# Performance work log

Hardware: AMD Instinct MI355X
Metric: run time of the kernel (lower is better)

Reference implementation:

```python
import jax, jax.numpy as jnp
import numpy as np

N, E, DIM, H, T, R = 50000, 400000, 128, 8, 4, 6
D = DIM // H  # head dim = 16


def setup_inputs() -> dict:
    key = jax.random.key(0)
    ks = jax.random.split(key, 12)
    s = 0.1
    return {
        "x": jax.random.normal(ks[0], (N, DIM), jnp.float32),
        "src": jax.random.randint(ks[1], (E,), 0, N),
        "dst": jax.random.randint(ks[2], (E,), 0, N),
        "ntype": jax.random.randint(ks[3], (N,), 0, T),
        "etype": jax.random.randint(ks[4], (E,), 0, R),
        # TypedLinear weights: [num_types, in, out] (no bias in DGL TypedLinear)
        "Wk": jax.random.normal(ks[5], (T, DIM, DIM), jnp.float32) * s,
        "Wq": jax.random.normal(ks[6], (T, DIM, DIM), jnp.float32) * s,
        "Wv": jax.random.normal(ks[7], (T, DIM, DIM), jnp.float32) * s,
        "Wa": jax.random.normal(ks[8], (T, DIM, DIM), jnp.float32) * s,
        # relation_pri[h][r], relation_att/msg: per-head per-etype [D,D]
        "rel_pri": jnp.ones((H, R), jnp.float32) + jax.random.normal(ks[9], (H, R), jnp.float32) * 0.1,
        "rel_att": jax.random.normal(ks[10], (H, R, D, D), jnp.float32) * 0.25,
        "rel_msg": jax.random.normal(ks[11], (H, R, D, D), jnp.float32) * 0.25,
        "skip": jnp.ones((T,), jnp.float32),  # sigmoid-gated skip per node type
        "ln_gamma": jnp.ones((DIM,), jnp.float32),
        "ln_beta": jnp.zeros((DIM,), jnp.float32),
    }


def _typed_linear(x, W, types):
    # x: [N, in], W: [Ttypes, in, out], types: [N] -> y_i = x_i @ W[types_i]
    out = jnp.zeros((x.shape[0], W.shape[-1]), x.dtype)
    for t in range(W.shape[0]):
        out = jnp.where((types == t)[:, None], x @ W[t], out)
    return out


def _typed_rel(xe, W, etype):
    # xe: [E, H, D], W: [H, Rtypes, D, D] -> y_e[h] = xe_e[h] @ W[h, etype_e]
    out = jnp.zeros_like(xe)
    for r in range(W.shape[1]):
        yr = jnp.einsum('ehd,hdo->eho', xe, W[:, r])
        out = jnp.where((etype == r)[:, None, None], yr, out)
    return out


def reference(x, src, dst, ntype, etype, Wk, Wq, Wv, Wa, rel_pri, rel_att, rel_msg, skip, ln_gamma, ln_beta):
    # ---- HGTConv ----
    k = _typed_linear(x, Wk, ntype).reshape(N, H, D)
    q = _typed_linear(x, Wq, ntype).reshape(N, H, D)
    v = _typed_linear(x, Wv, ntype).reshape(N, H, D)
    k_e = k[src]   # [E,H,D]
    q_e = q[dst]
    v_e = v[src]
    kw = _typed_rel(k_e, rel_att, etype)                       # [E,H,D]
    a = (kw * q_e).sum(-1) * rel_pri.T[etype] / jnp.sqrt(jnp.float32(D))  # [E,H]
    m = _typed_rel(v_e, rel_msg, etype)                        # [E,H,D]
    # edge softmax over incoming edges per dst node, per head
    amax = jax.lax.stop_gradient(jax.ops.segment_max(a, dst, num_segments=N))
    amax = jnp.where(jnp.isfinite(amax), amax, 0.0)
    ex = jnp.exp(a - amax[dst])
    den = jax.ops.segment_sum(ex, dst, num_segments=N)
    attn = ex / jnp.maximum(den[dst], 1e-9)                    # [E,H]
    h = jax.ops.segment_sum(m * attn[:, :, None], dst, num_segments=N).reshape(N, DIM)
    h = _typed_linear(h, Wa, ntype)  # dropout = identity (eval mode)
    gate = jax.nn.sigmoid(skip)[ntype][:, None]
    h = h * gate + x * (1.0 - gate)  # in_dim == out_dim -> identity skip path
    # ---- RelationAwareLayer tail: Identity residual + dropout(identity) + LayerNorm ----
    y = x + h
    mu = y.mean(-1, keepdims=True)
    var = ((y - mu) ** 2).mean(-1, keepdims=True)
    return (y - mu) / jnp.sqrt(var + 1e-5) * ln_gamma + ln_beta
```

## Files before the change

### kernel.cpp

```cpp
#include <hip/hip_runtime.h>
#include <math.h>

#define N_NODES 50000
#define N_EDGES 400000
#define H_HEADS 8
#define D_HEAD 16
#define R_TYPES 6
#define T_TYPES 4
#define DIM 128
#define BN 16
#define MAX_TILES ((N_NODES + BN - 1) / BN + T_TYPES)
#define NKEYS (N_NODES * R_TYPES)
#define NBLK_K ((NKEYS + 255) / 256)
#define NBLK_N ((N_NODES + 255) / 256)
#define SM_SHIFT 8.0f

typedef unsigned short bf16_t;

__device__ __forceinline__ float bf2f(bf16_t u) {
    unsigned int v = ((unsigned int)u) << 16;
    return __int_as_float((int)v);
}
__device__ __forceinline__ bf16_t f2bf(float f) {
    unsigned int u = (unsigned int)__float_as_int(f);
    unsigned int lsb = (u >> 16) & 1u;
    u += 0x7fffu + lsb;
    return (bf16_t)(u >> 16);
}
__device__ __forceinline__ void bf2x(unsigned int u, float& a, float& b) {
    a = bf2f((bf16_t)(u & 0xffffu));
    b = bf2f((bf16_t)(u >> 16));
}
__device__ __forceinline__ unsigned int pk(float a, float b) {
    return (unsigned int)f2bf(a) | ((unsigned int)f2bf(b) << 16);
}


__global__ void k_scanA(const int* __restrict__ cnt, int* __restrict__ offs,
                        int* __restrict__ partial, int n) {
    __shared__ int tmp[256];
    int tid = threadIdx.x;
    int i = blockIdx.x * 256 + tid;
    int v = (i < n) ? cnt[i] : 0;
    tmp[tid] = v;
    __syncthreads();
    for (int o = 1; o < 256; o <<= 1) {
        int t = (tid >= o) ? tmp[tid - o] : 0;
        __syncthreads();
        tmp[tid] += t;
        __syncthreads();
    }
    if (i < n) offs[i] = tmp[tid] - v;
    if (tid == 255) partial[blockIdx.x] = tmp[255];
}

__global__ void k_rscan(int* __restrict__ a, int total) {
    __shared__ int tmp[256];
    __shared__ int carry_s;
    int tid = threadIdx.x;
    if (tid == 0) carry_s = 0;
    __syncthreads();
    for (int base = 0; base < total; base += 256) {
        int i = base + tid;
        int v = (i < total) ? a[i] : 0;
        tmp[tid] = v;
        __syncthreads();
        for (int o = 1; o < 256; o <<= 1) {
            int t = (tid >= o) ? tmp[tid - o] : 0;
            __syncthreads();
            tmp[tid] += t;
            __syncthreads();
        }
        int carry = carry_s;
        if (i < total) a[i] = carry + tmp[tid] - v;
        __syncthreads();
        if (tid == 255) carry_s = carry + tmp[255];
        __syncthreads();
    }
}

__global__ void k_scanC2(int* __restrict__ offs, const int* __restrict__ partial,
                         int* __restrict__ cursor, int n) {
    int i = blockIdx.x * 256 + threadIdx.x;
    if (i < n) {
        int v = offs[i] + partial[blockIdx.x];
        offs[i] = v;
        cursor[i] = v;
    }
}


__global__ void k_count6(const int* __restrict__ srcA, const int* __restrict__ etype,
                         int* __restrict__ deg6, int n) {
    int e = blockIdx.x * blockDim.x + threadIdx.x;
    if (e < n) atomicAdd(&deg6[etype[e] * N_NODES + srcA[e]], 1);
}

__global__ void k_countD(const int* __restrict__ dst, int* __restrict__ degD, int n) {
    int e = blockIdx.x * blockDim.x + threadIdx.x;
    if (e < n) atomicAdd(&degD[dst[e]], 1);
}

__global__ void k_scatter6(const int* __restrict__ src, const int* __restrict__ dst,
                           const int* __restrict__ etype, int* __restrict__ cursor6,
                           int* __restrict__ esrc_s, int* __restrict__ edst_s, int n) {
    int e = blockIdx.x * blockDim.x + threadIdx.x;
    if (e < n) {
        int key = etype[e] * N_NODES + src[e];
        int pos = atomicAdd(&cursor6[key], 1);
        esrc_s[pos] = src[e];
        edst_s[pos] = dst[e];
    }
}

__global__ void k_dpos(const int* __restrict__ edst_s, int* __restrict__ cursorD,
                       int* __restrict__ dpos, int n) {
    int p = blockIdx.x * blockDim.x + threadIdx.x;
    if (p < n) dpos[p] = atomicAdd(&cursorD[edst_s[p]], 1);
}


__global__ void k_tcount_agg(const int* __restrict__ ntype, int* __restrict__ tcnt,
                             int* __restrict__ wpos, int n) {
    __shared__ int hist[T_TYPES];
    __shared__ int base[T_TYPES];
    int tid = threadIdx.x;
    if (tid < T_TYPES) hist[tid] = 0;
    __syncthreads();
    int i = blockIdx.x * 256 + tid;
    int t = 0, rank = 0;
    if (i < n) {
        t = ntype[i];
        rank = atomicAdd(&hist[t], 1);
    }
    __syncthreads();
    if (tid < T_TYPES)
        base[tid] = (hist[tid] > 0) ? atomicAdd(&tcnt[tid], hist[tid]) : 0;
    __syncthreads();
    if (i < n) wpos[i] = base[t] + rank;
}

__global__ void k_tsetup(const int* __restrict__ tcnt, int* __restrict__ pbase,
                         int* __restrict__ ntiles_g, int* __restrict__ tile_type) {
    __shared__ int off[T_TYPES + 1];
    if (threadIdx.x == 0) {
        int o = 0;
        for (int t = 0; t < T_TYPES; ++t) {
            off[t] = o;
            pbase[t] = o * BN;
            o += (tcnt[t] + BN - 1) / BN;
        }
        off[T_TYPES] = o;
        *ntiles_g = o;
    }
    __syncthreads();
    int total = off[T_TYPES];
    for (int i = threadIdx.x; i < total; i += blockDim.x) {
        int t = 0;
        while (t < T_TYPES - 1 && i >= off[t + 1]) ++t;
        tile_type[i] = t;
    }
}

__global__ void k_tscatter2(const int* __restrict__ ntype, const int* __restrict__ wpos,
                            const int* __restrict__ pbase, int* __restrict__ nlist, int n) {
    int i = blockIdx.x * 256 + threadIdx.x;
    if (i < n) nlist[pbase[ntype[i]] + wpos[i]] = i;
}


__global__ __launch_bounds__(192) void k_kqv_gemm4(
    const float* __restrict__ x, const int* __restrict__ nlist,
    const int* __restrict__ tile_type, const int* __restrict__ ntiles_g,
    const float* __restrict__ Wk, const float* __restrict__ Wq,
    const float* __restrict__ Wv,
    bf16_t* __restrict__ kb, bf16_t* __restrict__ qb, bf16_t* __restrict__ vb) {
    __shared__ float xs[BN][DIM];
    __shared__ int sids[BN];
    int b = blockIdx.x;
    if (b >= *ntiles_g) return;
    int tid = threadIdx.x;
    if (tid < BN) sids[tid] = nlist[b * BN + tid];
    __syncthreads();
    for (int idx = tid; idx < BN * (DIM / 4); idx += 192) {
        int row = idx >> 5;
        int q4 = idx & 31;
        int nid = sids[row];
        float4 v4 = make_float4(0.f, 0.f, 0.f, 0.f);
        if (nid >= 0) v4 = *(const float4*)(x + (size_t)nid * DIM + q4 * 4);
        *(float4*)(&xs[row][q4 * 4]) = v4;
    }
    __syncthreads();
    int lt = tid / 96;
    int wi = tid % 96;
    int mat = wi >> 5;
    int colq = wi & 31;
    int t = tile_type[b];
    const float* W = (mat == 0 ? Wk : (mat == 1 ? Wq : Wv))
                     + (size_t)t * DIM * DIM + colq * 4;
    float acc[8][4];
#pragma unroll
    for (int n = 0; n < 8; ++n) {
        acc[n][0] = 0.f; acc[n][1] = 0.f; acc[n][2] = 0.f; acc[n][3] = 0.f;
    }
    const float* xbase = &xs[lt * 8][0];
    for (int dq = 0; dq < 32; ++dq) {
        float4 w0 = *(const float4*)(W + (size_t)(dq * 4 + 0) * DIM);
        float4 w1 = *(const float4*)(W + (size_t)(dq * 4 + 1) * DIM);
        float4 w2 = *(const float4*)(W + (size_t)(dq * 4 + 2) * DIM);
        float4 w3 = *(const float4*)(W + (size_t)(dq * 4 + 3) * DIM);
#pragma unroll
        for (int n = 0; n < 8; ++n) {
            float4 xv = *(const float4*)(xbase + n * DIM + dq * 4);
            acc[n][0] = fmaf(xv.x, w0.x, acc[n][0]);
            acc[n][0] = fmaf(xv.y, w1.x, acc[n][0]);
            acc[n][0] = fmaf(xv.z, w2.x, acc[n][0]);
            acc[n][0] = fmaf(xv.w, w3.x, acc[n][0]);
            acc[n][1] = fmaf(xv.x, w0.y, acc[n][1]);
            acc[n][1] = fmaf(xv.y, w1.y, acc[n][1]);
            acc[n][1] = fmaf(xv.z, w2.y, acc[n][1]);
            acc[n][1] = fmaf(xv.w, w3.y, acc[n][1]);
            acc[n][2] = fmaf(xv.x, w0.z, acc[n][2]);
            acc[n][2] = fmaf(xv.y, w1.z, acc[n][2]);
            acc[n][2] = fmaf(xv.z, w2.z, acc[n][2]);
            acc[n][2] = fmaf(xv.w, w3.z, acc[n][2]);
            acc[n][3] = fmaf(xv.x, w0.w, acc[n][3]);
            acc[n][3] = fmaf(xv.y, w1.w, acc[n][3]);
            acc[n][3] = fmaf(xv.z, w2.w, acc[n][3]);
            acc[n][3] = fmaf(xv.w, w3.w, acc[n][3]);
        }
    }
    bf16_t* ob = (mat == 0 ? kb : (mat == 1 ? qb : vb));
#pragma unroll
    for (int n = 0; n < 8; ++n) {
        int nid = sids[lt * 8 + n];
        if (nid >= 0) {
            ushort4 o4;
            o4.x = f2bf(acc[n][0]); o4.y = f2bf(acc[n][1]);
            o4.z = f2bf(acc[n][2]); o4.w = f2bf(acc[n][3]);
            *(ushort4*)(ob + (size_t)nid * DIM + colq * 4) = o4;
        }
    }
}


__global__ __launch_bounds__(256) void k_edge_m(
    const bf16_t* __restrict__ kbuf, const bf16_t* __restrict__ qbuf,
    const bf16_t* __restrict__ vbuf,
    const int* __restrict__ esrc_s, const int* __restrict__ edst_s,
    const int* __restrict__ beg6, const int* __restrict__ dpos,
    const float* __restrict__ rel_att, const float* __restrict__ rel_msg,
    const float* __restrict__ rel_pri,
    float* __restrict__ ex_out, bf16_t* __restrict__ m_out, int nE) {
    __shared__ float A2[2][8 * 260];
    __shared__ float M2[2][8 * 260];
    __shared__ float pri[2][8];
    __shared__ int rb_s[R_TYPES + 1];
    __shared__ int r01[2];
    int b = blockIdx.x;
    int e0 = b * 32;
    int tid = threadIdx.x;
    int nHere = nE - e0; if (nHere > 32) nHere = 32;
    if (nHere <= 0) return;
    if (tid < R_TYPES) rb_s[tid] = beg6[tid * N_NODES];
    if (tid == R_TYPES) rb_s[R_TYPES] = nE;
    __syncthreads();
    if (tid == 0) {
        int rA = 0, rB = 0;
        int eL = e0 + nHere - 1;
#pragma unroll
        for (int r = 1; r < R_TYPES; ++r) {
            if (e0 >= rb_s[r]) rA = r;
            if (eL >= rb_s[r]) rB = r;
        }
        r01[0] = rA; r01[1] = rB;
    }
    __syncthreads();
    int r0 = r01[0], r1 = r01[1];
    int bnd = rb_s[r0 + 1];
    for (int idx = tid; idx < 2 * 2048; idx += 256) {
        int slot = idx >> 11;
        if (slot == 1 && r1 == r0) break;
        int rem = idx & 2047;
        int h = rem >> 8, dj = rem & 255;
        int rr = slot ? r1 : r0;
        A2[slot][h * 260 + dj] = rel_att[(h * R_TYPES + rr) * 256 + dj];
        M2[slot][h * 260 + dj] = rel_msg[(h * R_TYPES + rr) * 256 + dj];
    }
    if (tid < 16) {
        int slot = tid >> 3, h = tid & 7;
        pri[slot][h] = rel_pri[h * R_TYPES + (slot ? r1 : r0)] * 0.25f;
    }
    __syncthreads();
    int el = tid >> 3;
    int h  = tid & 7;
    int q2 = e0 + el;
    if (q2 >= nE) return;
    int s = esrc_s[q2], dn = edst_s[q2];
    int slot = (q2 >= bnd) ? 1 : 0;
    const uint4* kp = (const uint4*)(kbuf + (size_t)s  * DIM + h * 16);
    const uint4* qp = (const uint4*)(qbuf + (size_t)dn * DIM + h * 16);
    const uint4* vp = (const uint4*)(vbuf + (size_t)s  * DIM + h * 16);
    uint4 ka = kp[0], kb4 = kp[1];
    uint4 qa = qp[0], qb4 = qp[1];
    uint4 va = vp[0], vb4 = vp[1];
    float kk[16], qq[16], vv[16];
    bf2x(ka.x,  kk[0],  kk[1]);  bf2x(ka.y,  kk[2],  kk[3]);
    bf2x(ka.z,  kk[4],  kk[5]);  bf2x(ka.w,  kk[6],  kk[7]);
    bf2x(kb4.x, kk[8],  kk[9]);  bf2x(kb4.y, kk[10], kk[11]);
    bf2x(kb4.z, kk[12], kk[13]); bf2x(kb4.w, kk[14], kk[15]);
    bf2x(qa.x,  qq[0],  qq[1]);  bf2x(qa.y,  qq[2],  qq[3]);
    bf2x(qa.z,  qq[4],  qq[5]);  bf2x(qa.w,  qq[6],  qq[7]);
    bf2x(qb4.x, qq[8],  qq[9]);  bf2x(qb4.y, qq[10], qq[11]);
    bf2x(qb4.z, qq[12], qq[13]); bf2x(qb4.w, qq[14], qq[15]);
    bf2x(va.x,  vv[0],  vv[1]);  bf2x(va.y,  vv[2],  vv[3]);
    bf2x(va.z,  vv[4],  vv[5]);  bf2x(va.w,  vv[6],  vv[7]);
    bf2x(vb4.x, vv[8],  vv[9]);  bf2x(vb4.y, vv[10], vv[11]);
    bf2x(vb4.z, vv[12], vv[13]); bf2x(vb4.w, vv[14], vv[15]);

    const float4* A4 = (const float4*)&A2[slot][h * 260];
    float accj[16];
#pragma unroll
    for (int j = 0; j < 16; ++j) accj[j] = 0.f;
#pragma unroll
    for (int d = 0; d < 16; ++d) {
        float kd = kk[d];
#pragma unroll
        for (int jj = 0; jj < 4; ++jj) {
            float4 a4 = A4[d * 4 + jj];
            accj[jj * 4 + 0] = fmaf(kd, a4.x, accj[jj * 4 + 0]);
            accj[jj * 4 + 1] = fmaf(kd, a4.y, accj[jj * 4 + 1]);
            accj[jj * 4 + 2] = fmaf(kd, a4.z, accj[jj * 4 + 2]);
            accj[jj * 4 + 3] = fmaf(kd, a4.w, accj[jj * 4 + 3]);
        }
    }
    float a = 0.f;
#pragma unroll
    for (int j = 0; j < 16; ++j) a = fmaf(accj[j], qq[j], a);
    float ex = __expf(a * pri[slot][h] - SM_SHIFT);

    const float4* M4 = (const float4*)&M2[slot][h * 260];
    float mj[16];
#pragma unroll
    for (int j = 0; j < 16; ++j) mj[j] = 0.f;
#pragma unroll
    for (int d = 0; d < 16; ++d) {
        float vd = vv[d];
#pragma unroll
        for (int jj = 0; jj < 4; ++jj) {
            float4 m4 = M4[d * 4 + jj];
            mj[jj * 4 + 0] = fmaf(vd, m4.x, mj[jj * 4 + 0]);
            mj[jj * 4 + 1] = fmaf(vd, m4.y, mj[jj * 4 + 1]);
            mj[jj * 4 + 2] = fmaf(vd, m4.z, mj[jj * 4 + 2]);
            mj[jj * 4 + 3] = fmaf(vd, m4.w, mj[jj * 4 + 3]);
        }
    }
    int dp = dpos[q2];
    ex_out[(size_t)dp * 8 + h] = ex;
    uint4 o0, o1;
    o0.x = pk(ex * mj[0],  ex * mj[1]);  o0.y = pk(ex * mj[2],  ex * mj[3]);
    o0.z = pk(ex * mj[4],  ex * mj[5]);  o0.w = pk(ex * mj[6],  ex * mj[7]);
    o1.x = pk(ex * mj[8],  ex * mj[9]);  o1.y = pk(ex * mj[10], ex * mj[11]);
    o1.z = pk(ex * mj[12], ex * mj[13]); o1.w = pk(ex * mj[14], ex * mj[15]);
    uint4* op = (uint4*)(m_out + (size_t)dp * DIM + h * 16);
    op[0] = o0; op[1] = o1;
}


__global__ __launch_bounds__(256) void k_agg_stream(
    const bf16_t* __restrict__ m_out, const float* __restrict__ ex_out,
    const int* __restrict__ doffD, const int* __restrict__ degD,
    float* __restrict__ hacc, int n) {
    int tid = threadIdx.x;
    int nb = tid >> 7;
    int lane2 = tid & 127;
    int node = blockIdx.x * 2 + nb;
    if (node >= n) return;
    int h = lane2 >> 4;
    int off = doffD[node];
    int dg  = degD[node];
    float acc = 0.f, den = 0.f;
#pragma unroll 4
    for (int j = 0; j < dg; ++j) {
        den += ex_out[(size_t)(off + j) * 8 + h];
        acc += bf2f(m_out[(size_t)(off + j) * DIM + lane2]);
    }
    hacc[(size_t)node * DIM + lane2] = acc / fmaxf(den, 1e-9f);
}


__global__ __launch_bounds__(256) void k_final_gemm(
    const float* __restrict__ x, const int* __restrict__ nlist,
    const int* __restrict__ tile_type, const int* __restrict__ ntiles_g,
    const float* __restrict__ Wa, const float* __restrict__ skip,
    const float* __restrict__ gamma, const float* __restrict__ beta,
    float* __restrict__ out) {
    __shared__ float hs[BN][DIM];
    __shared__ float ys[BN][DIM];
    __shared__ int sids[BN];
    __shared__ float mred[BN], ired[BN];
    int b = blockIdx.x;
    if (b >= *ntiles_g) return;
    int tid = threadIdx.x;
    if (tid < BN) sids[tid] = nlist[b * BN + tid];
    __syncthreads();
    for (int idx = tid; idx < BN * DIM; idx += 256) {
        int row = idx >> 7, col = idx & 127;
        int nid = sids[row];
        hs[row][col] = (nid >= 0) ? out[(size_t)nid * DIM + col] : 0.f;
    }
    __syncthreads();
    int t = tile_type[b];
    int half = tid >> 7, col = tid & 127;
    const float* W = Wa + (size_t)t * DIM * DIM;
    float acc[8];
#pragma unroll
    for (int n = 0; n < 8; ++n) acc[n] = 0.f;
#pragma unroll 4
    for (int d = 0; d < DIM; ++d) {
        float w = W[d * DIM + col];
#pragma unroll
        for (int n = 0; n < 8; ++n) acc[n] = fmaf(hs[half * 8 + n][d], w, acc[n]);
    }
    float gte = 1.f / (1.f + __expf(-skip[t]));
#pragma unroll
    for (int n = 0; n < 8; ++n) {
        int row = half * 8 + n;
        int nid = sids[row];
        float xv = (nid >= 0) ? x[(size_t)nid * DIM + col] : 0.f;
        ys[row][col] = xv * (2.f - gte) + acc[n] * gte;
    }
    __syncthreads();
    int ng = tid >> 4, l16 = tid & 15;
    float s = 0.f, s2 = 0.f;
#pragma unroll
    for (int k2 = 0; k2 < 8; ++k2) {
        float yv = ys[ng][l16 + 16 * k2];
        s += yv; s2 += yv * yv;
    }
#pragma unroll
    for (int m = 1; m < 16; m <<= 1) {
        s  += __shfl_xor(s, m, 64);
        s2 += __shfl_xor(s2, m, 64);
    }
    if (l16 == 0) {
        float mu = s * (1.f / DIM);
        float var = s2 * (1.f / DIM) - mu * mu;
        mred[ng] = mu;
        ired[ng] = rsqrtf(var + 1e-5f);
    }
    __syncthreads();
    float gm = gamma[col], bt = beta[col];
#pragma unroll
    for (int n = 0; n < 8; ++n) {
        int row = half * 8 + n;
        int nid = sids[row];
        if (nid >= 0)
            out[(size_t)nid * DIM + col] = (ys[row][col] - mred[row]) * ired[row] * gm + bt;
    }
}


extern "C" void kernel_launch(void* const* d_in, const int* in_sizes, int n_in,
                              void* d_out, int out_size, void* d_ws, size_t ws_size,
                              hipStream_t stream) {
    const float* x       = (const float*)d_in[0];
    const int*   src     = (const int*)d_in[1];
    const int*   dst     = (const int*)d_in[2];
    const int*   ntype   = (const int*)d_in[3];
    const int*   etype   = (const int*)d_in[4];
    const float* Wk      = (const float*)d_in[5];
    const float* Wq      = (const float*)d_in[6];
    const float* Wv      = (const float*)d_in[7];
    const float* Wa      = (const float*)d_in[8];
    const float* rel_pri = (const float*)d_in[9];
    const float* rel_att = (const float*)d_in[10];
    const float* rel_msg = (const float*)d_in[11];
    const float* skip    = (const float*)d_in[12];
    const float* gamma   = (const float*)d_in[13];
    const float* beta    = (const float*)d_in[14];
    float* out = (float*)d_out;

    const int N = N_NODES, E = N_EDGES;

    char* ws = (char*)d_ws;
    float* ex_out = (float*)ws;
    int* deg6    = (int*)(ex_out + (size_t)E * H_HEADS);
    int* beg6    = deg6 + NKEYS;
    int* cursor6 = beg6 + NKEYS;
    int* partial6 = cursor6 + NKEYS;
    int* degD    = partial6 + NBLK_K;
    int* doffD   = degD + N;
    int* cursorD = doffD + N;
    int* partialD = cursorD + N;
    int* dpos    = partialD + NBLK_N;
    int* esrc_s  = dpos + E;
    int* edst_s  = esrc_s + E;
    int* tcnt    = edst_s + E;
    int* pbase   = tcnt + T_TYPES;
    int* ntiles  = pbase + T_TYPES;
    int* tile_type = ntiles + 1;
    int* nlist   = tile_type + MAX_TILES;
    int* wpos    = nlist + (size_t)MAX_TILES * BN;
    bf16_t* kb   = (bf16_t*)(wpos + N);
    bf16_t* qb   = kb + (size_t)N * DIM;
    bf16_t* vb   = qb + (size_t)N * DIM;
    bf16_t* m_out = vb + (size_t)N * DIM;

    const int nbE = (E + 255) / 256;

    hipMemsetAsync(deg6, 0, (size_t)NKEYS * sizeof(int), stream);
    hipMemsetAsync(degD, 0, (size_t)N * sizeof(int), stream);
    k_count6<<<nbE, 256, 0, stream>>>(src, etype, deg6, E);
    k_countD<<<nbE, 256, 0, stream>>>(dst, degD, E);
    k_scanA<<<NBLK_K, 256, 0, stream>>>(deg6, beg6, partial6, NKEYS);
    k_rscan<<<1, 256, 0, stream>>>(partial6, NBLK_K);
    k_scanC2<<<NBLK_K, 256, 0, stream>>>(beg6, partial6, cursor6, NKEYS);
    k_scanA<<<NBLK_N, 256, 0, stream>>>(degD, doffD, partialD, N);
    k_rscan<<<1, 256, 0, stream>>>(partialD, NBLK_N);
    k_scanC2<<<NBLK_N, 256, 0, stream>>>(doffD, partialD, cursorD, N);
    k_scatter6<<<nbE, 256, 0, stream>>>(
        src, dst, etype, cursor6, esrc_s, edst_s, E);
    k_dpos<<<nbE, 256, 0, stream>>>(edst_s, cursorD, dpos, E);

    hipMemsetAsync(tcnt, 0, T_TYPES * sizeof(int), stream);
    k_tcount_agg<<<NBLK_N, 256, 0, stream>>>(ntype, tcnt, wpos, N);
    k_tsetup<<<1, 256, 0, stream>>>(tcnt, pbase, ntiles, tile_type);
    hipMemsetAsync(nlist, 0xFF, (size_t)MAX_TILES * BN * sizeof(int), stream);
    k_tscatter2<<<NBLK_N, 256, 0, stream>>>(ntype, wpos, pbase, nlist, N);

    k_kqv_gemm4<<<MAX_TILES, 192, 0, stream>>>(
        x, nlist, tile_type, ntiles, Wk, Wq, Wv, kb, qb, vb);

    k_edge_m<<<(E + 31) / 32, 256, 0, stream>>>(
        kb, qb, vb, esrc_s, edst_s, beg6, dpos,
        rel_att, rel_msg, rel_pri, ex_out, m_out, E);

    k_agg_stream<<<(N + 1) / 2, 256, 0, stream>>>(
        m_out, ex_out, doffD, degD, out, N);

    k_final_gemm<<<MAX_TILES, 256, 0, stream>>>(
        x, nlist, tile_type, ntiles, Wa, skip, gamma, beta, out);
}
```

Measured before the change: 387.5 us.

## Pad per-relation edge segments to 32 so each edge block has one relation

Edges sorted by relation type are now laid out with each relation's segment padded to a multiple of 32, so every 32-edge block in the edge kernel covers a single relation. This removes the dual-slot shared-memory staging of relation matrices, the boundary search against beg6, and the per-edge slot selection. In exchange it adds two small setup kernels, memsets of the padded index arrays, up to 192 extra padded slots, and guards on negative indices in the dpos and edge kernels.

Result: slower. 396.8 us (+2.4%).

```diff
diff --git a/kernel.cpp b/kernel.cpp
--- a/kernel.cpp
+++ b/kernel.cpp
@@ -13,6 +13,7 @@
 #define NKEYS (N_NODES * R_TYPES)
 #define NBLK_K ((NKEYS + 255) / 256)
 #define NBLK_N ((N_NODES + 255) / 256)
+#define EPAD_MAX (N_EDGES + R_TYPES * 32)
 #define SM_SHIFT 8.0f
 
 typedef unsigned short bf16_t;
@@ -79,6 +80,11 @@
     }
 }
 
+__global__ void k_scanC(int* __restrict__ offs, const int* __restrict__ partial, int n) {
+    int i = blockIdx.x * 256 + threadIdx.x;
+    if (i < n) offs[i] += partial[blockIdx.x];
+}
+
 __global__ void k_scanC2(int* __restrict__ offs, const int* __restrict__ partial,
                          int* __restrict__ cursor, int n) {
     int i = blockIdx.x * 256 + threadIdx.x;
@@ -99,6 +105,30 @@
 __global__ void k_countD(const int* __restrict__ dst, int* __restrict__ degD, int n) {
     int e = blockIdx.x * blockDim.x + threadIdx.x;
     if (e < n) atomicAdd(&degD[dst[e]], 1);
+}
+
+__global__ void k_padsetup(const int* __restrict__ beg6, int* __restrict__ rb_pad,
+                           int* __restrict__ rstart, int nE) {
+    if (threadIdx.x == 0 && blockIdx.x == 0) {
+        int o = 0;
+        for (int r = 0; r < R_TYPES; ++r) {
+            int st = beg6[r * N_NODES];
+            rstart[r] = st;
+            int en = (r < R_TYPES - 1) ? beg6[(r + 1) * N_NODES] : nE;
+            rb_pad[r] = o;
+            o += (en - st + 31) & ~31;
+        }
+        rb_pad[R_TYPES] = o;
+    }
+}
+
+__global__ void k_cursor_pad(const int* __restrict__ beg6, const int* __restrict__ rb_pad,
+                             const int* __restrict__ rstart, int* __restrict__ cursor6, int n) {
+    int i = blockIdx.x * 256 + threadIdx.x;
+    if (i < n) {
+        int r = i / N_NODES;
+        cursor6[i] = rb_pad[r] + (beg6[i] - rstart[r]);
+    }
 }
 
 __global__ void k_scatter6(const int* __restrict__ src, const int* __restrict__ dst,
@@ -116,7 +146,10 @@
 __global__ void k_dpos(const int* __restrict__ edst_s, int* __restrict__ cursorD,
                        int* __restrict__ dpos, int n) {
     int p = blockIdx.x * blockDim.x + threadIdx.x;
-    if (p < n) dpos[p] = atomicAdd(&cursorD[edst_s[p]], 1);
+    if (p < n) {
+        int dn = edst_s[p];
+        if (dn >= 0) dpos[p] = atomicAdd(&cursorD[dn], 1);
+    }
 }
 
 
@@ -244,60 +277,42 @@
 }
 
 
-__global__ __launch_bounds__(256) void k_edge_m(
+__global__ __launch_bounds__(256) void k_edge_m2(
     const bf16_t* __restrict__ kbuf, const bf16_t* __restrict__ qbuf,
     const bf16_t* __restrict__ vbuf,
     const int* __restrict__ esrc_s, const int* __restrict__ edst_s,
-    const int* __restrict__ beg6, const int* __restrict__ dpos,
+    const int* __restrict__ rb_pad, const int* __restrict__ dpos,
     const float* __restrict__ rel_att, const float* __restrict__ rel_msg,
     const float* __restrict__ rel_pri,
-    float* __restrict__ ex_out, bf16_t* __restrict__ m_out, int nE) {
-    __shared__ float A2[2][8 * 260];
-    __shared__ float M2[2][8 * 260];
-    __shared__ float pri[2][8];
-    __shared__ int rb_s[R_TYPES + 1];
-    __shared__ int r01[2];
+    float* __restrict__ ex_out, bf16_t* __restrict__ m_out) {
+    __shared__ float A2[8 * 260];
+    __shared__ float M2[8 * 260];
+    __shared__ float pri[8];
+    __shared__ int r_s;
     int b = blockIdx.x;
     int e0 = b * 32;
     int tid = threadIdx.x;
-    int nHere = nE - e0; if (nHere > 32) nHere = 32;
-    if (nHere <= 0) return;
-    if (tid < R_TYPES) rb_s[tid] = beg6[tid * N_NODES];
-    if (tid == R_TYPES) rb_s[R_TYPES] = nE;
-    __syncthreads();
     if (tid == 0) {
-        int rA = 0, rB = 0;
-        int eL = e0 + nHere - 1;
-#pragma unroll
-        for (int r = 1; r < R_TYPES; ++r) {
-            if (e0 >= rb_s[r]) rA = r;
-            if (eL >= rb_s[r]) rB = r;
-        }
-        r01[0] = rA; r01[1] = rB;
-    }
-    __syncthreads();
-    int r0 = r01[0], r1 = r01[1];
-    int bnd = rb_s[r0 + 1];
-    for (int idx = tid; idx < 2 * 2048; idx += 256) {
-        int slot = idx >> 11;
-        if (slot == 1 && r1 == r0) break;
-        int rem = idx & 2047;
-        int h = rem >> 8, dj = rem & 255;
-        int rr = slot ? r1 : r0;
-        A2[slot][h * 260 + dj] = rel_att[(h * R_TYPES + rr) * 256 + dj];
-        M2[slot][h * 260 + dj] = rel_msg[(h * R_TYPES + rr) * 256 + dj];
-    }
-    if (tid < 16) {
-        int slot = tid >> 3, h = tid & 7;
-        pri[slot][h] = rel_pri[h * R_TYPES + (slot ? r1 : r0)] * 0.25f;
-    }
+        int r = 0;
+#pragma unroll
+        for (int q = 1; q < R_TYPES; ++q) if (e0 >= rb_pad[q]) r = q;
+        r_s = r;
+    }
+    __syncthreads();
+    int r = r_s;
+    for (int idx = tid; idx < 2048; idx += 256) {
+        int h = idx >> 8, dj = idx & 255;
+        A2[h * 260 + dj] = rel_att[(h * R_TYPES + r) * 256 + dj];
+        M2[h * 260 + dj] = rel_msg[(h * R_TYPES + r) * 256 + dj];
+    }
+    if (tid < 8) pri[tid] = rel_pri[tid * R_TYPES + r] * 0.25f;
     __syncthreads();
     int el = tid >> 3;
     int h  = tid & 7;
     int q2 = e0 + el;
-    if (q2 >= nE) return;
-    int s = esrc_s[q2], dn = edst_s[q2];
-    int slot = (q2 >= bnd) ? 1 : 0;
+    int s = esrc_s[q2];
+    if (s < 0) return;
+    int dn = edst_s[q2];
     const uint4* kp = (const uint4*)(kbuf + (size_t)s  * DIM + h * 16);
     const uint4* qp = (const uint4*)(qbuf + (size_t)dn * DIM + h * 16);
     const uint4* vp = (const uint4*)(vbuf + (size_t)s  * DIM + h * 16);
@@ -318,7 +333,7 @@
     bf2x(vb4.x, vv[8],  vv[9]);  bf2x(vb4.y, vv[10], vv[11]);
     bf2x(vb4.z, vv[12], vv[13]); bf2x(vb4.w, vv[14], vv[15]);
 
-    const float4* A4 = (const float4*)&A2[slot][h * 260];
+    const float4* A4 = (const float4*)&A2[h * 260];
     float accj[16];
 #pragma unroll
     for (int j = 0; j < 16; ++j) accj[j] = 0.f;
@@ -337,9 +352,9 @@
     float a = 0.f;
 #pragma unroll
     for (int j = 0; j < 16; ++j) a = fmaf(accj[j], qq[j], a);
-    float ex = __expf(a * pri[slot][h] - SM_SHIFT);
-
-    const float4* M4 = (const float4*)&M2[slot][h * 260];
+    float ex = __expf(a * pri[h] - SM_SHIFT);
+
+    const float4* M4 = (const float4*)&M2[h * 260];
     float mj[16];
 #pragma unroll
     for (int j = 0; j < 16; ++j) mj[j] = 0.f;
@@ -493,10 +508,12 @@
     int* doffD   = degD + N;
     int* cursorD = doffD + N;
     int* partialD = cursorD + N;
-    int* dpos    = partialD + NBLK_N;
-    int* esrc_s  = dpos + E;
-    int* edst_s  = esrc_s + E;
-    int* tcnt    = edst_s + E;
+    int* rb_pad  = partialD + NBLK_N;
+    int* rstart  = rb_pad + R_TYPES + 1;
+    int* dpos    = rstart + R_TYPES;
+    int* esrc_s  = dpos + EPAD_MAX;
+    int* edst_s  = esrc_s + EPAD_MAX;
+    int* tcnt    = edst_s + EPAD_MAX;
     int* pbase   = tcnt + T_TYPES;
     int* ntiles  = pbase + T_TYPES;
     int* tile_type = ntiles + 1;
@@ -508,20 +525,25 @@
     bf16_t* m_out = vb + (size_t)N * DIM;
 
     const int nbE = (E + 255) / 256;
+    const int nbEP = (EPAD_MAX + 255) / 256;
 
     hipMemsetAsync(deg6, 0, (size_t)NKEYS * sizeof(int), stream);
     hipMemsetAsync(degD, 0, (size_t)N * sizeof(int), stream);
+    hipMemsetAsync(esrc_s, 0xFF, (size_t)EPAD_MAX * sizeof(int), stream);
+    hipMemsetAsync(edst_s, 0xFF, (size_t)EPAD_MAX * sizeof(int), stream);
     k_count6<<<nbE, 256, 0, stream>>>(src, etype, deg6, E);
     k_countD<<<nbE, 256, 0, stream>>>(dst, degD, E);
     k_scanA<<<NBLK_K, 256, 0, stream>>>(deg6, beg6, partial6, NKEYS);
     k_rscan<<<1, 256, 0, stream>>>(partial6, NBLK_K);
-    k_scanC2<<<NBLK_K, 256, 0, stream>>>(beg6, partial6, cursor6, NKEYS);
+    k_scanC<<<NBLK_K, 256, 0, stream>>>(beg6, partial6, NKEYS);
+    k_padsetup<<<1, 64, 0, stream>>>(beg6, rb_pad, rstart, E);
+    k_cursor_pad<<<NBLK_K, 256, 0, stream>>>(beg6, rb_pad, rstart, cursor6, NKEYS);
     k_scanA<<<NBLK_N, 256, 0, stream>>>(degD, doffD, partialD, N);
     k_rscan<<<1, 256, 0, stream>>>(partialD, NBLK_N);
     k_scanC2<<<NBLK_N, 256, 0, stream>>>(doffD, partialD, cursorD, N);
     k_scatter6<<<nbE, 256, 0, stream>>>(
         src, dst, etype, cursor6, esrc_s, edst_s, E);
-    k_dpos<<<nbE, 256, 0, stream>>>(edst_s, cursorD, dpos, E);
+    k_dpos<<<nbEP, 256, 0, stream>>>(edst_s, cursorD, dpos, EPAD_MAX);
 
     hipMemsetAsync(tcnt, 0, T_TYPES * sizeof(int), stream);
     k_tcount_agg<<<NBLK_N, 256, 0, stream>>>(ntype, tcnt, wpos, N);
@@ -532,9 +554,9 @@
     k_kqv_gemm4<<<MAX_TILES, 192, 0, stream>>>(
         x, nlist, tile_type, ntiles, Wk, Wq, Wv, kb, qb, vb);
 
-    k_edge_m<<<(E + 31) / 32, 256, 0, stream>>>(
-        kb, qb, vb, esrc_s, edst_s, beg6, dpos,
-        rel_att, rel_msg, rel_pri, ex_out, m_out, E);
+    k_edge_m2<<<EPAD_MAX / 32, 256, 0, stream>>>(
+        kb, qb, vb, esrc_s, edst_s, rb_pad, dpos,
+        rel_att, rel_msg, rel_pri, ex_out, m_out);
 
     k_agg_stream<<<(N + 1) / 2, 256, 0, stream>>>(
         m_out, ex_out, doffD, degD, out, N);
```
